# Kernel optimization log

Measured on AMD Instinct MI355X. Metric: run time of the kernel, lower is better.

## Reference

```python
import jax, jax.numpy as jnp
import numpy as np

DK, DV, NH = 512, 256, 8  # matches init_kwargs


def rel_to_abs(x):
    # x: (B, N, L, 2L-1) -> (B, N, L, L) via pad/reshape trick
    B, N, L, _ = x.shape
    x = jnp.pad(x, ((0, 0), (0, 0), (0, 0), (0, 1)))          # (B,N,L,2L)
    x = x.reshape(B, N, L * 2 * L)
    x = jnp.pad(x, ((0, 0), (0, 0), (0, L - 1)))
    x = x.reshape(B, N, L + 1, 2 * L - 1)
    return x[:, :, :L, L - 1:]


def relative_logits_1d(q, rel_k):
    # q: (B, nh, A, Wd, dkh); rel_k: (dkh, 2*Wd-1)
    B, nh, A, Wd, _ = q.shape
    rel = jnp.einsum('bnawc,cm->bnawm', q, rel_k)             # (B,nh,A,Wd,2Wd-1)
    rel = rel.reshape(B, nh * A, Wd, 2 * Wd - 1)
    rel = rel_to_abs(rel).reshape(B, nh, A, 1, Wd, Wd)
    return jnp.broadcast_to(rel, (B, nh, A, A, Wd, Wd))


def reference(x, w_qkv, w_conv, w_out, key_rel_h, key_rel_w):
    B, Cin, H, W = x.shape
    dkh, dvh = DK // NH, DV // NH
    L = H * W
    # 1x1 qkv projection (stride 1)
    qkv = jnp.einsum('bchw,oc->bohw', x, w_qkv)               # (B, 2dk+dv, H, W)
    q = qkv[:, :DK]
    k = qkv[:, DK:2 * DK]
    v = qkv[:, 2 * DK:]
    flat_q = q.reshape(B, NH, dkh, L) * (dkh ** -0.5)
    flat_k = k.reshape(B, NH, dkh, L)
    flat_v = v.reshape(B, NH, dvh, L)
    logits = jnp.einsum('bncs,bnct->bnst', flat_q, flat_k)     # (B,nh,L,L)
    # relative position logits (uses the already-scaled q, as in the torch code)
    qr = flat_q.reshape(B, NH, dkh, H, W).transpose(0, 1, 3, 4, 2)  # (B,nh,H,W,dkh)
    w_rel = relative_logits_1d(qr, key_rel_w)                  # (B,nh,H,H,W,W)
    h_rel = relative_logits_1d(qr.transpose(0, 1, 3, 2, 4), key_rel_h)  # (B,nh,W,W,H,H)
    h_rel = h_rel.transpose(0, 1, 2, 4, 3, 5).reshape(B, NH, L, L)
    w_rel = w_rel.transpose(0, 1, 4, 2, 5, 3).reshape(B, NH, L, L)
    logits = logits + h_rel + w_rel
    weights = jax.nn.softmax(logits, axis=-1)
    attn = jnp.einsum('bnst,bnct->bnsc', weights, flat_v)      # (B,nh,L,dvh)
    attn = attn.transpose(0, 1, 3, 2).reshape(B, DV, H, W)
    attn = jnp.einsum('bchw,oc->bohw', attn, w_out)            # 1x1 out_proj
    conv_out = jax.lax.conv_general_dilated(
        x, w_conv, window_strides=(1, 1), padding=[(1, 1), (1, 1)],
        dimension_numbers=('NCHW', 'OIHW', 'NCHW'))            # (B, out_c-dv, H, W)
    return jnp.concatenate([conv_out, attn], axis=1)


def setup_inputs() -> dict:
    key = jax.random.key(0)
    ks = jax.random.split(key, 6)
    H, W, Cin = 32, 32, 256
    return {
        'x': jax.random.normal(ks[0], (8, Cin, H, W), jnp.float32),
        'w_qkv': jax.random.normal(ks[1], (2 * DK + DV, Cin), jnp.float32) * 0.02,
        'w_conv': jax.random.normal(ks[2], (256, Cin, 3, 3), jnp.float32) * 0.02,
        'w_out': jax.random.normal(ks[3], (DV, DV), jnp.float32) * 0.02,
        'key_rel_h': DK ** -0.5 + jax.random.normal(ks[4], (DK // NH, 2 * H - 1), jnp.float32),
        'key_rel_w': DK ** -0.5 + jax.random.normal(ks[5], (DK // NH, 2 * W - 1), jnp.float32),
    }
```

## Files before the change

### kernel.cpp

```cpp
#include <hip/hip_runtime.h>
#include <cstddef>
#include <cstdint>

#define NB 8
#define CIN 256
#define LL 1024
#define DKC 512
#define DVC 256
#define XPSTRIDE 295936

typedef short short8 __attribute__((ext_vector_type(8)));
typedef float f32x4 __attribute__((ext_vector_type(4)));

__device__ __forceinline__ unsigned short f2bf(float f) {
  unsigned int u = __float_as_uint(f);
  u += 0x7fffu + ((u >> 16) & 1u);
  return (unsigned short)(u >> 16);
}
__device__ __forceinline__ float bf2f(unsigned short u) {
  return __uint_as_float(((unsigned int)u) << 16);
}

__global__ __launch_bounds__(256) void prep_weights(
    const float* __restrict__ wconv, const float* __restrict__ wqkv,
    const float* __restrict__ wout, const float* __restrict__ krh,
    const float* __restrict__ krw, unsigned short* __restrict__ wtap,
    unsigned short* __restrict__ wqbf, unsigned short* __restrict__ woutbf,
    unsigned short* __restrict__ relTh, unsigned short* __restrict__ relTw,
    unsigned short* __restrict__ xTp) {
  const int idx = blockIdx.x * 256 + threadIdx.x;
  if (idx < 589824) {
    const int g = idx >> 14;
    const int ot = g / 9, tap = g - ot * 9;
    const int rem2 = idx & 16383;
    const int kc = rem2 >> 12;
    const int row = (rem2 >> 6) & 63, kin = rem2 & 63;
    const int o = ot * 64 + row, c = kc * 64 + kin;
    wtap[idx] = f2bf(wconv[(size_t)(o * 256 + c) * 9 + tap]);
  } else if (idx < 917504) {
    const int j = idx - 589824;
    const int g = j >> 12;
    const int ot = g >> 2, kc = g & 3;
    const int row = (j >> 6) & 63, kin = j & 63;
    const int o = ot * 64 + row, c = kc * 64 + kin;
    const float sc = (o < DKC) ? 0.125f * 1.44269504088896f : 1.0f;
    wqbf[j] = f2bf(wqkv[o * 256 + c] * sc);
  } else if (idx < 983040) {
    const int j = idx - 917504;
    const int g = j >> 12;
    const int o = (g >> 2) * 64 + ((j >> 6) & 63);
    const int c = (g & 3) * 64 + (j & 63);
    woutbf[j] = f2bf(wout[o * 256 + c]);
  } else if (idx < 991232) {
    const int j = idx - 983040;
    const int tbl = j >> 12;
    const int rest = j & 4095;
    const int m = rest >> 6, c = rest & 63;
    const float* src = tbl ? krw : krh;
    unsigned short* dst = tbl ? relTw : relTh;
    const float v = (m < 63) ? src[c * 63 + m] : 0.f;
    dst[m * 64 + c] = f2bf(v);
  } else {
    const int j2 = idx - 991232;
    const int b = j2 / 33792;
    const int rem = j2 - b * 33792;
    const int pos = rem >> 8, c = rem & 255;
    int hp, wp;
    if (pos < 34) { hp = 0; wp = pos; }
    else if (pos < 68) { hp = 33; wp = pos - 34; }
    else if (pos < 100) { hp = pos - 68 + 1; wp = 0; }
    else { hp = pos - 100 + 1; wp = 33; }
    xTp[(size_t)b * XPSTRIDE + (hp * 34 + wp) * 256 + c] = 0;
  }
}

__global__ __launch_bounds__(256) void xpad_interior(
    const float* __restrict__ x, unsigned short* __restrict__ xTp) {
  __shared__ float tile[64][65];
  const int st = blockIdx.x;
  const int b = blockIdx.y;
  const int s0 = st * 64;
  const int h0 = st * 2;
  const int tid = threadIdx.x;
  for (int cc = 0; cc < 4; ++cc) {
    const int c0 = cc * 64;
    {
      const int row = tid >> 2;
      const int j0 = (tid & 3) * 16;
#pragma unroll
      for (int k = 0; k < 4; ++k)
        *(float4*)&tile[row][j0 + k * 4] =
            *(const float4*)(x + ((size_t)(b * CIN + c0 + row)) * LL + s0 + j0 + k * 4);
    }
    __syncthreads();
    {
      const int sl = tid >> 2;
      const int cb = (tid & 3) * 16;
      unsigned short buf[16];
#pragma unroll
      for (int m = 0; m < 16; ++m) buf[m] = f2bf(tile[cb + m][sl]);
      const int hp = h0 + (sl >> 5) + 1;
      const int wp = (sl & 31) + 1;
      unsigned short* dst = xTp + (size_t)b * XPSTRIDE + (hp * 34 + wp) * 256 + c0 + cb;
      *(uint4*)dst = *(uint4*)&buf[0];
      *(uint4*)(dst + 8) = *(uint4*)&buf[8];
    }
    __syncthreads();
  }
}

__global__ __launch_bounds__(256) void qkv_mfma(
    const unsigned short* __restrict__ xTp, const unsigned short* __restrict__ wqbf,
    unsigned short* __restrict__ qbf, unsigned short* __restrict__ kbf,
    unsigned short* __restrict__ vbf) {
  __shared__ __align__(16) char qsmem[16640];
  unsigned short* bs = (unsigned short*)qsmem;
  float (*trans)[65] = (float(*)[65])qsmem;
  const int tid = threadIdx.x;
  const int lane = tid & 63, w = tid >> 6;
  const int n16 = lane & 15, quad = lane >> 4;
  const int ot = blockIdx.x;
  const int st = blockIdx.y;
  const int b = blockIdx.z;
  const int s0 = st * 64;
  const int h0 = st * 2;
  const int trow = tid >> 3, ck = tid & 7;

  const unsigned short* xb = xTp + (size_t)b * XPSTRIDE;
  const unsigned short* wA = wqbf + (size_t)ot * 16384 + (w * 16 + n16) * 64 + quad * 8;
  const int wpos = (trow & 31) + 1;

  f32x4 acc[4];
#pragma unroll
  for (int nt = 0; nt < 4; ++nt) acc[nt] = (f32x4){0.f, 0.f, 0.f, 0.f};

  uint4 rb0 = *(const uint4*)(xb + (size_t)((h0 + 1) * 34 + wpos) * 256 + ck * 8);
  uint4 rb1 = *(const uint4*)(xb + (size_t)((h0 + 2) * 34 + wpos) * 256 + ck * 8);
  short8 af0 = *(const short8*)(wA);
  short8 af1 = *(const short8*)(wA + 32);
#pragma unroll
  for (int kc = 0; kc < 4; ++kc) {
    __syncthreads();
    *(uint4*)&bs[trow * 64 + ((ck ^ (trow & 7)) * 8)] = rb0;
    *(uint4*)&bs[(trow + 32) * 64 + ((ck ^ (trow & 7)) * 8)] = rb1;
    __syncthreads();
    short8 a0 = af0, a1 = af1;
    if (kc < 3) {
      const int c0 = (kc + 1) * 64;
      rb0 = *(const uint4*)(xb + (size_t)((h0 + 1) * 34 + wpos) * 256 + c0 + ck * 8);
      rb1 = *(const uint4*)(xb + (size_t)((h0 + 2) * 34 + wpos) * 256 + c0 + ck * 8);
      af0 = *(const short8*)(wA + (kc + 1) * 4096);
      af1 = *(const short8*)(wA + (kc + 1) * 4096 + 32);
    }
#pragma unroll
    for (int nt = 0; nt < 4; ++nt) {
      short8 b0 = *(const short8*)&bs[(nt * 16 + n16) * 64 + ((quad ^ (n16 & 7)) * 8)];
      short8 b1 = *(const short8*)&bs[(nt * 16 + n16) * 64 + (((quad + 4) ^ (n16 & 7)) * 8)];
      acc[nt] = __builtin_amdgcn_mfma_f32_16x16x32_bf16(a0, b0, acc[nt], 0, 0, 0);
      acc[nt] = __builtin_amdgcn_mfma_f32_16x16x32_bf16(a1, b1, acc[nt], 0, 0, 0);
    }
  }
  __syncthreads();
#pragma unroll
  for (int nt = 0; nt < 4; ++nt)
#pragma unroll
    for (int reg = 0; reg < 4; ++reg)
      trans[w * 16 + quad * 4 + reg][nt * 16 + n16] = acc[nt][reg];
  __syncthreads();
  const int sl = tid >> 2;
  const int cseg = (tid & 3) * 16;
  unsigned short buf[16];
  if (ot < 16) {
#pragma unroll
    for (int m = 0; m < 16; ++m) buf[m] = f2bf(trans[cseg + m][sl]);
    unsigned short* dst;
    int head;
    if (ot < 8) { dst = qbf; head = ot; }
    else { dst = kbf; head = ot - 8; }
    const size_t base = (((size_t)(b * 8 + head)) * LL + s0 + sl) * 64 + cseg;
    *(uint4*)(dst + base) = *(uint4*)&buf[0];
    *(uint4*)(dst + base + 8) = *(uint4*)&buf[8];
  } else {
#pragma unroll
    for (int m = 0; m < 16; ++m) buf[m] = f2bf(trans[sl][cseg + m]);
    unsigned short* dst = vbf + ((size_t)b * DVC + (ot - 16) * 64 + sl) * LL + s0 + cseg;
    *(uint4*)dst = *(uint4*)&buf[0];
    *(uint4*)(dst + 8) = *(uint4*)&buf[8];
  }
}

__global__ __launch_bounds__(256) void conv_mfma(
    const unsigned short* __restrict__ xTp, const unsigned short* __restrict__ wtap,
    float* __restrict__ out) {
  __shared__ __align__(16) unsigned short bs[64 * 64];
  const int tid = threadIdx.x;
  const int lane = tid & 63, w = tid >> 6;
  const int n16 = lane & 15, quad = lane >> 4;
  const int ot = blockIdx.x;
  const int st = blockIdx.y;
  const int b = blockIdx.z;
  const int s0 = st * 64;
  const int h0 = st * 2;
  const int trow = tid >> 3;
  const int ck = tid & 7;

  const unsigned short* xb = xTp + (size_t)b * XPSTRIDE;
  const unsigned short* wA = wtap + (size_t)ot * 147456 + (w * 16 + n16) * 64 + quad * 8;

  f32x4 acc[4];
#pragma unroll
  for (int nt = 0; nt < 4; ++nt) acc[nt] = (f32x4){0.f, 0.f, 0.f, 0.f};

  uint4 rb0, rb1;
  auto loadB = [&](int it) {
    const int tap = it >> 2;
    const int c0 = (it & 3) * 64;
    const int dh = tap / 3 - 1;
    const int dw = tap - (tap / 3) * 3 - 1;
    const int wp = (trow & 31) + dw + 1;
    rb0 = *(const uint4*)(xb + (size_t)((h0 + dh + 1) * 34 + wp) * 256 + c0 + ck * 8);
    rb1 = *(const uint4*)(xb + (size_t)((h0 + dh + 2) * 34 + wp) * 256 + c0 + ck * 8);
  };
  loadB(0);
  short8 af0 = *(const short8*)(wA);
  short8 af1 = *(const short8*)(wA + 32);
  for (int it = 0; it < 36; ++it) {
    __syncthreads();
    *(uint4*)&bs[trow * 64 + ((ck ^ (trow & 7)) * 8)] = rb0;
    *(uint4*)&bs[(trow + 32) * 64 + ((ck ^ (trow & 7)) * 8)] = rb1;
    __syncthreads();
    short8 a0 = af0, a1 = af1;
    if (it < 35) {
      loadB(it + 1);
      af0 = *(const short8*)(wA + (size_t)(it + 1) * 4096);
      af1 = *(const short8*)(wA + (size_t)(it + 1) * 4096 + 32);
    }
#pragma unroll
    for (int nt = 0; nt < 4; ++nt) {
      short8 b0 = *(const short8*)&bs[(nt * 16 + n16) * 64 + ((quad ^ (n16 & 7)) * 8)];
      short8 b1 = *(const short8*)&bs[(nt * 16 + n16) * 64 + (((quad + 4) ^ (n16 & 7)) * 8)];
      acc[nt] = __builtin_amdgcn_mfma_f32_16x16x32_bf16(a0, b0, acc[nt], 0, 0, 0);
      acc[nt] = __builtin_amdgcn_mfma_f32_16x16x32_bf16(a1, b1, acc[nt], 0, 0, 0);
    }
  }
#pragma unroll
  for (int nt = 0; nt < 4; ++nt)
#pragma unroll
    for (int reg = 0; reg < 4; ++reg)
      out[((size_t)b * 512 + ot * 64 + w * 16 + quad * 4 + reg) * LL + s0 + nt * 16 + n16] =
          acc[nt][reg];
}

__global__ __launch_bounds__(256, 4) void attn_kernel(
    const unsigned short* __restrict__ qbf, const unsigned short* __restrict__ kbf,
    const unsigned short* __restrict__ vbf, const unsigned short* __restrict__ relTh,
    const unsigned short* __restrict__ relTw, unsigned short* __restrict__ abf) {
  __shared__ __align__(16) char smem[28672];
  unsigned short* ks = (unsigned short*)smem;
  unsigned short* vs = (unsigned short*)(smem + 8192);
  unsigned short* ps = (unsigned short*)(smem + 12288);
  unsigned short* rwtT = (unsigned short*)(smem + 20480);
  float* obuf = (float*)smem;

  const int tid = threadIdx.x;
  const int lane = tid & 63, w = tid >> 6;
  const int n16 = lane & 15, quad = lane >> 4;
  const int blk = blockIdx.x;
  const int bn = blk & 63, qb = blk >> 6;
  const int n = bn & 7, b = bn >> 3;
  const int s0 = qb * 64;
  const int aa = 2 * qb + (w >> 1);
  const int pb = (w & 1) * 16;

  const unsigned short* qbase = qbf + ((size_t)(b * 8 + n)) * LL * 64;
  const unsigned short* kbase = kbf + ((size_t)(b * 8 + n)) * LL * 64;
  const unsigned short* vbase = vbf + ((size_t)(b * 8 + n)) * 32 * LL;

  const int ck = tid & 7;
  const int trow = tid >> 3;

  uint4 pk0 = *(const uint4*)(kbase + trow * 64 + ck * 8);
  uint4 pk1 = *(const uint4*)(kbase + (trow + 32) * 64 + ck * 8);
  uint4 pv = *(const uint4*)(vbase + (size_t)trow * LL + ck * 8);

  {
    const int sT = (pb + n16) * 32 + aa;
    short8 ra0 = *(const short8*)(qbase + (size_t)sT * 64 + quad * 8);
    short8 ra1 = *(const short8*)(qbase + (size_t)sT * 64 + 32 + quad * 8);
#pragma unroll
    for (int tbl = 0; tbl < 2; ++tbl) {
      const unsigned short* rel = tbl ? relTh : relTw;
      f32x4 acc[4];
#pragma unroll
      for (int mt = 0; mt < 4; ++mt) acc[mt] = (f32x4){0.f, 0.f, 0.f, 0.f};
#pragma unroll
      for (int mt = 0; mt < 4; ++mt) {
        short8 b0 = *(const short8*)(rel + (mt * 16 + n16) * 64 + quad * 8);
        short8 b1 = *(const short8*)(rel + (mt * 16 + n16) * 64 + 32 + quad * 8);
        acc[mt] = __builtin_amdgcn_mfma_f32_16x16x32_bf16(ra0, b0, acc[mt], 0, 0, 0);
        acc[mt] = __builtin_amdgcn_mfma_f32_16x16x32_bf16(ra1, b1, acc[mt], 0, 0, 0);
      }
      if (tbl == 0) {
#pragma unroll
        for (int mt = 0; mt < 4; ++mt)
#pragma unroll
          for (int reg = 0; reg < 4; ++reg)
            rwtT[(mt * 16 + n16) * 64 +
                 ((w * 16 + quad * 4 + reg) ^ ((n16 & 7) * 8))] = f2bf(acc[mt][reg]);
      } else {
#pragma unroll
        for (int mt = 0; mt < 4; ++mt)
#pragma unroll
          for (int reg = 0; reg < 4; ++reg)
            ps[(w * 16 + quad * 4 + reg) * 64 + mt * 16 + n16] = f2bf(acc[mt][reg]);
      }
    }
  }
  short8 qf0 = *(const short8*)(qbase + (size_t)(s0 + w * 16 + n16) * 64 + quad * 8);
  short8 qf1 = *(const short8*)(qbase + (size_t)(s0 + w * 16 + n16) * 64 + 32 + quad * 8);
  __syncthreads();
  float rhreg[2][4];
#pragma unroll
  for (int tt1 = 0; tt1 < 2; ++tt1)
#pragma unroll
    for (int reg = 0; reg < 4; ++reg) {
      const int iL = quad * 4 + reg;
      rhreg[tt1][reg] = bf2f(ps[(w * 16 + iL) * 64 + tt1 * 16 + n16 + 31 - pb - iL]);
    }

  float lacc[4] = {0.f, 0.f, 0.f, 0.f};
  f32x4 oacc[2];
  oacc[0] = (f32x4){0.f, 0.f, 0.f, 0.f};
  oacc[1] = (f32x4){0.f, 0.f, 0.f, 0.f};

  unsigned short* psw = ps + w * 1024;
  const int rb = w * 16 + quad * 4;

  for (int kt64 = 0; kt64 < 16; ++kt64) {
    const int t0 = kt64 * 64;
    __syncthreads();
    *(uint4*)&ks[trow * 64 + ((ck ^ (trow & 7)) * 8)] = pk0;
    *(uint4*)&ks[(trow + 32) * 64 + ((ck ^ (trow & 7)) * 8)] = pk1;
    *(uint4*)&vs[trow * 64 + ((ck ^ (trow & 7)) * 8)] = pv;
    __syncthreads();
    if (kt64 < 15) {
      const unsigned short* kg = kbase + (size_t)(t0 + 64) * 64;
      pk0 = *(const uint4*)(kg + trow * 64 + ck * 8);
      pk1 = *(const uint4*)(kg + (trow + 32) * 64 + ck * 8);
      pv = *(const uint4*)(vbase + (size_t)trow * LL + t0 + 64 + ck * 8);
    }

    f32x4 sacc[4];
#pragma unroll
    for (int tt = 0; tt < 4; ++tt) sacc[tt] = (f32x4){0.f, 0.f, 0.f, 0.f};
#pragma unroll
    for (int tt = 0; tt < 4; ++tt) {
      short8 kb0 = *(const short8*)&ks[(tt * 16 + n16) * 64 + ((quad ^ (n16 & 7)) * 8)];
      short8 kb1 = *(const short8*)&ks[(tt * 16 + n16) * 64 + (((quad + 4) ^ (n16 & 7)) * 8)];
      sacc[tt] = __builtin_amdgcn_mfma_f32_16x16x32_bf16(qf0, kb0, sacc[tt], 0, 0, 0);
      sacc[tt] = __builtin_amdgcn_mfma_f32_16x16x32_bf16(qf1, kb1, sacc[tt], 0, 0, 0);
    }
    float rwv[2][4];
#pragma unroll
    for (int h = 0; h < 2; ++h) {
      const int mw = (t0 >> 5) + h - aa + 31;
      const ushort4 rw4 = *(const ushort4*)&rwtT[mw * 64 + (rb ^ ((mw & 7) * 8))];
      rwv[h][0] = bf2f(rw4.x); rwv[h][1] = bf2f(rw4.y);
      rwv[h][2] = bf2f(rw4.z); rwv[h][3] = bf2f(rw4.w);
    }
#pragma unroll
    for (int tt = 0; tt < 4; ++tt)
#pragma unroll
      for (int reg = 0; reg < 4; ++reg) {
        const float e =
            __builtin_amdgcn_exp2f(sacc[tt][reg] + rwv[tt >> 1][reg] + rhreg[tt & 1][reg]);
        lacc[reg] += e;
        const int r = quad * 4 + reg;
        psw[r * 64 + (((tt * 2 + (n16 >> 3)) ^ (r & 7)) * 8) + (n16 & 7)] =
            (unsigned short)(__float_as_uint(e) >> 16);
      }
    __asm__ volatile("s_waitcnt lgkmcnt(0)" ::: "memory");
#pragma unroll
    for (int kt = 0; kt < 2; ++kt) {
      short8 pa = *(const short8*)&psw[n16 * 64 + (((quad + 4 * kt) ^ (n16 & 7)) * 8)];
#pragma unroll
      for (int ct = 0; ct < 2; ++ct) {
        short8 vb = *(const short8*)&vs[(ct * 16 + n16) * 64 + (((quad + 4 * kt) ^ (n16 & 7)) * 8)];
        oacc[ct] = __builtin_amdgcn_mfma_f32_16x16x32_bf16(pa, vb, oacc[ct], 0, 0, 0);
      }
    }
  }
  float linv[4];
#pragma unroll
  for (int reg = 0; reg < 4; ++reg) {
    float l = lacc[reg];
#pragma unroll
    for (int m = 1; m < 16; m <<= 1) l += __shfl_xor(l, m, 16);
    linv[reg] = 1.0f / l;
  }
  __syncthreads();
#pragma unroll
  for (int ct = 0; ct < 2; ++ct)
#pragma unroll
    for (int reg = 0; reg < 4; ++reg)
      obuf[(w * 16 + quad * 4 + reg) * 33 + ct * 16 + n16] = oacc[ct][reg] * linv[reg];
  __syncthreads();
  {
    const int row = tid >> 2;
    const int cseg = (tid & 3) * 8;
    unsigned short buf8[8];
#pragma unroll
    for (int m = 0; m < 8; ++m) buf8[m] = f2bf(obuf[row * 33 + cseg + m]);
    *(uint4*)(abf + (((size_t)b * LL) + s0 + row) * 256 + n * 32 + cseg) = *(uint4*)&buf8[0];
  }
}

__global__ __launch_bounds__(256) void proj_mfma(
    const unsigned short* __restrict__ abf, const unsigned short* __restrict__ woutbf,
    float* __restrict__ out) {
  __shared__ __align__(16) unsigned short bs[64 * 64];
  const int tid = threadIdx.x;
  const int lane = tid & 63, w = tid >> 6;
  const int n16 = lane & 15, quad = lane >> 4;
  const int ot = blockIdx.x;
  const int st = blockIdx.y;
  const int b = blockIdx.z;
  const int s0 = st * 64;
  const int trow = tid >> 3, ck = tid & 7;

  const unsigned short* ab = abf + ((size_t)b * LL + s0) * 256;
  const unsigned short* wA = woutbf + (size_t)ot * 16384 + (w * 16 + n16) * 64 + quad * 8;

  f32x4 acc[4];
#pragma unroll
  for (int nt = 0; nt < 4; ++nt) acc[nt] = (f32x4){0.f, 0.f, 0.f, 0.f};

  uint4 rb0 = *(const uint4*)(ab + (size_t)trow * 256 + ck * 8);
  uint4 rb1 = *(const uint4*)(ab + (size_t)(trow + 32) * 256 + ck * 8);
  short8 af0 = *(const short8*)(wA);
  short8 af1 = *(const short8*)(wA + 32);
#pragma unroll
  for (int kc = 0; kc < 4; ++kc) {
    __syncthreads();
    *(uint4*)&bs[trow * 64 + ((ck ^ (trow & 7)) * 8)] = rb0;
    *(uint4*)&bs[(trow + 32) * 64 + ((ck ^ (trow & 7)) * 8)] = rb1;
    __syncthreads();
    short8 a0 = af0, a1 = af1;
    if (kc < 3) {
      const int c0 = (kc + 1) * 64;
      rb0 = *(const uint4*)(ab + (size_t)trow * 256 + c0 + ck * 8);
      rb1 = *(const uint4*)(ab + (size_t)(trow + 32) * 256 + c0 + ck * 8);
      af0 = *(const short8*)(wA + (kc + 1) * 4096);
      af1 = *(const short8*)(wA + (kc + 1) * 4096 + 32);
    }
#pragma unroll
    for (int nt = 0; nt < 4; ++nt) {
      short8 b0 = *(const short8*)&bs[(nt * 16 + n16) * 64 + ((quad ^ (n16 & 7)) * 8)];
      short8 b1 = *(const short8*)&bs[(nt * 16 + n16) * 64 + (((quad + 4) ^ (n16 & 7)) * 8)];
      acc[nt] = __builtin_amdgcn_mfma_f32_16x16x32_bf16(a0, b0, acc[nt], 0, 0, 0);
      acc[nt] = __builtin_amdgcn_mfma_f32_16x16x32_bf16(a1, b1, acc[nt], 0, 0, 0);
    }
  }
#pragma unroll
  for (int nt = 0; nt < 4; ++nt)
#pragma unroll
    for (int reg = 0; reg < 4; ++reg)
      out[((size_t)b * 512 + 256 + ot * 64 + w * 16 + quad * 4 + reg) * LL + s0 + nt * 16 + n16] =
          acc[nt][reg];
}

extern "C" void kernel_launch(void* const* d_in, const int* in_sizes, int n_in,
                              void* d_out, int out_size, void* d_ws, size_t ws_size,
                              hipStream_t stream) {
  const float* x     = (const float*)d_in[0];
  const float* wqkv  = (const float*)d_in[1];
  const float* wconv = (const float*)d_in[2];
  const float* wout  = (const float*)d_in[3];
  const float* krh   = (const float*)d_in[4];
  const float* krw   = (const float*)d_in[5];
  float* out = (float*)d_out;

  unsigned short* qbf = (unsigned short*)d_ws;
  unsigned short* kbf = qbf + (size_t)NB * 8 * LL * 64;
  unsigned short* vbf = kbf + (size_t)NB * 8 * LL * 64;
  unsigned short* abf = vbf + (size_t)NB * DVC * LL;
  unsigned short* relTh = abf + (size_t)NB * LL * DVC;
  unsigned short* relTw = relTh + 4096;
  unsigned short* xTp = relTw + 4096;
  unsigned short* wtap = xTp + (size_t)NB * XPSTRIDE;
  unsigned short* wqbf = wtap + 589824;
  unsigned short* woutbf = wqbf + 327680;

  prep_weights<<<dim3(4928), 256, 0, stream>>>(wconv, wqkv, wout, krh, krw,
                                               wtap, wqbf, woutbf, relTh, relTw, xTp);
  xpad_interior<<<dim3(16, 8), 256, 0, stream>>>(x, xTp);
  qkv_mfma<<<dim3(20, 16, NB), 256, 0, stream>>>(xTp, wqbf, qbf, kbf, vbf);
  conv_mfma<<<dim3(4, 16, NB), 256, 0, stream>>>(xTp, wtap, out);
  attn_kernel<<<dim3(1024), 256, 0, stream>>>(qbf, kbf, vbf, relTh, relTw, abf);
  proj_mfma<<<dim3(4, 16, NB), 256, 0, stream>>>(abf, woutbf, out);
}
```

Measured before the change: 162.7 us.

## Double attention query tile per block and merge input prep kernels

Each attention block now handles 128 query rows instead of 64. K/V tiles loaded into shared memory are reused across two row sets, and the grid shrinks to 512 blocks. Shared memory grows and the occupancy hint drops from 4 to 2 blocks per CU, trading parallelism and registers for fewer K/V reloads. Separately, the x padding/transpose kernel is folded into the weight prep kernel to save one launch.

```diff
diff --git a/kernel.cpp b/kernel.cpp
--- a/kernel.cpp
+++ b/kernel.cpp
@@ -21,14 +21,48 @@
   return __uint_as_float(((unsigned int)u) << 16);
 }
 
-__global__ __launch_bounds__(256) void prep_weights(
-    const float* __restrict__ wconv, const float* __restrict__ wqkv,
-    const float* __restrict__ wout, const float* __restrict__ krh,
-    const float* __restrict__ krw, unsigned short* __restrict__ wtap,
-    unsigned short* __restrict__ wqbf, unsigned short* __restrict__ woutbf,
-    unsigned short* __restrict__ relTh, unsigned short* __restrict__ relTw,
-    unsigned short* __restrict__ xTp) {
-  const int idx = blockIdx.x * 256 + threadIdx.x;
+__global__ __launch_bounds__(256) void prep_all(
+    const float* __restrict__ x, const float* __restrict__ wconv,
+    const float* __restrict__ wqkv, const float* __restrict__ wout,
+    const float* __restrict__ krh, const float* __restrict__ krw,
+    unsigned short* __restrict__ wtap, unsigned short* __restrict__ wqbf,
+    unsigned short* __restrict__ woutbf, unsigned short* __restrict__ relTh,
+    unsigned short* __restrict__ relTw, unsigned short* __restrict__ xTp) {
+  __shared__ float tile[64][65];
+  const int tid = threadIdx.x;
+  if (blockIdx.x < 128) {
+    const int st = blockIdx.x & 15;
+    const int b = blockIdx.x >> 4;
+    const int s0 = st * 64;
+    const int h0 = st * 2;
+    for (int cc = 0; cc < 4; ++cc) {
+      const int c0 = cc * 64;
+      {
+        const int row = tid >> 2;
+        const int j0 = (tid & 3) * 16;
+#pragma unroll
+        for (int k = 0; k < 4; ++k)
+          *(float4*)&tile[row][j0 + k * 4] =
+              *(const float4*)(x + ((size_t)(b * CIN + c0 + row)) * LL + s0 + j0 + k * 4);
+      }
+      __syncthreads();
+      {
+        const int sl = tid >> 2;
+        const int cb = (tid & 3) * 16;
+        unsigned short buf[16];
+#pragma unroll
+        for (int m = 0; m < 16; ++m) buf[m] = f2bf(tile[cb + m][sl]);
+        const int hp = h0 + (sl >> 5) + 1;
+        const int wp = (sl & 31) + 1;
+        unsigned short* dst = xTp + (size_t)b * XPSTRIDE + (hp * 34 + wp) * 256 + c0 + cb;
+        *(uint4*)dst = *(uint4*)&buf[0];
+        *(uint4*)(dst + 8) = *(uint4*)&buf[8];
+      }
+      __syncthreads();
+    }
+    return;
+  }
+  const int idx = (blockIdx.x - 128) * 256 + tid;
   if (idx < 589824) {
     const int g = idx >> 14;
     const int ot = g / 9, tap = g - ot * 9;
@@ -74,41 +108,6 @@
   }
 }
 
-__global__ __launch_bounds__(256) void xpad_interior(
-    const float* __restrict__ x, unsigned short* __restrict__ xTp) {
-  __shared__ float tile[64][65];
-  const int st = blockIdx.x;
-  const int b = blockIdx.y;
-  const int s0 = st * 64;
-  const int h0 = st * 2;
-  const int tid = threadIdx.x;
-  for (int cc = 0; cc < 4; ++cc) {
-    const int c0 = cc * 64;
-    {
-      const int row = tid >> 2;
-      const int j0 = (tid & 3) * 16;
-#pragma unroll
-      for (int k = 0; k < 4; ++k)
-        *(float4*)&tile[row][j0 + k * 4] =
-            *(const float4*)(x + ((size_t)(b * CIN + c0 + row)) * LL + s0 + j0 + k * 4);
-    }
-    __syncthreads();
-    {
-      const int sl = tid >> 2;
-      const int cb = (tid & 3) * 16;
-      unsigned short buf[16];
-#pragma unroll
-      for (int m = 0; m < 16; ++m) buf[m] = f2bf(tile[cb + m][sl]);
-      const int hp = h0 + (sl >> 5) + 1;
-      const int wp = (sl & 31) + 1;
-      unsigned short* dst = xTp + (size_t)b * XPSTRIDE + (hp * 34 + wp) * 256 + c0 + cb;
-      *(uint4*)dst = *(uint4*)&buf[0];
-      *(uint4*)(dst + 8) = *(uint4*)&buf[8];
-    }
-    __syncthreads();
-  }
-}
-
 __global__ __launch_bounds__(256) void qkv_mfma(
     const unsigned short* __restrict__ xTp, const unsigned short* __restrict__ wqbf,
     unsigned short* __restrict__ qbf, unsigned short* __restrict__ kbf,
@@ -251,26 +250,26 @@
           acc[nt][reg];
 }
 
-__global__ __launch_bounds__(256, 4) void attn_kernel(
+__global__ __launch_bounds__(256, 2) void attn_kernel(
     const unsigned short* __restrict__ qbf, const unsigned short* __restrict__ kbf,
     const unsigned short* __restrict__ vbf, const unsigned short* __restrict__ relTh,
     const unsigned short* __restrict__ relTw, unsigned short* __restrict__ abf) {
-  __shared__ __align__(16) char smem[28672];
+  __shared__ __align__(16) char smem[45056];
   unsigned short* ks = (unsigned short*)smem;
   unsigned short* vs = (unsigned short*)(smem + 8192);
   unsigned short* ps = (unsigned short*)(smem + 12288);
-  unsigned short* rwtT = (unsigned short*)(smem + 20480);
+  unsigned short* rwtT = (unsigned short*)(smem + 28672);
   float* obuf = (float*)smem;
 
   const int tid = threadIdx.x;
   const int lane = tid & 63, w = tid >> 6;
   const int n16 = lane & 15, quad = lane >> 4;
   const int blk = blockIdx.x;
-  const int bn = blk & 63, qb = blk >> 6;
+  const int bn = blk & 63, qt = blk >> 6;
   const int n = bn & 7, b = bn >> 3;
-  const int s0 = qb * 64;
-  const int aa = 2 * qb + (w >> 1);
+  const int s0 = qt * 128;
   const int pb = (w & 1) * 16;
+  const int aar[2] = {4 * qt + (w >> 1), 4 * qt + 2 + (w >> 1)};
 
   const unsigned short* qbase = qbf + ((size_t)(b * 8 + n)) * LL * 64;
   const unsigned short* kbase = kbf + ((size_t)(b * 8 + n)) * LL * 64;
@@ -283,7 +282,9 @@
   uint4 pk1 = *(const uint4*)(kbase + (trow + 32) * 64 + ck * 8);
   uint4 pv = *(const uint4*)(vbase + (size_t)trow * LL + ck * 8);
 
-  {
+#pragma unroll
+  for (int rs = 0; rs < 2; ++rs) {
+    const int aa = aar[rs];
     const int sT = (pb + n16) * 32 + aa;
     short8 ra0 = *(const short8*)(qbase + (size_t)sT * 64 + quad * 8);
     short8 ra1 = *(const short8*)(qbase + (size_t)sT * 64 + 32 + quad * 8);
@@ -305,36 +306,45 @@
         for (int mt = 0; mt < 4; ++mt)
 #pragma unroll
           for (int reg = 0; reg < 4; ++reg)
-            rwtT[(mt * 16 + n16) * 64 +
-                 ((w * 16 + quad * 4 + reg) ^ ((n16 & 7) * 8))] = f2bf(acc[mt][reg]);
+            rwtT[(mt * 16 + n16) * 128 +
+                 ((rs * 64 + w * 16 + quad * 4 + reg) ^ ((n16 & 7) * 8))] = f2bf(acc[mt][reg]);
       } else {
 #pragma unroll
         for (int mt = 0; mt < 4; ++mt)
 #pragma unroll
           for (int reg = 0; reg < 4; ++reg)
-            ps[(w * 16 + quad * 4 + reg) * 64 + mt * 16 + n16] = f2bf(acc[mt][reg]);
-      }
-    }
-  }
-  short8 qf0 = *(const short8*)(qbase + (size_t)(s0 + w * 16 + n16) * 64 + quad * 8);
-  short8 qf1 = *(const short8*)(qbase + (size_t)(s0 + w * 16 + n16) * 64 + 32 + quad * 8);
+            ps[(rs * 64 + w * 16 + quad * 4 + reg) * 64 + mt * 16 + n16] = f2bf(acc[mt][reg]);
+      }
+    }
+  }
+  short8 qf[2][2];
+#pragma unroll
+  for (int rs = 0; rs < 2; ++rs) {
+    const size_t qrow = (size_t)(s0 + rs * 64 + w * 16 + n16) * 64;
+    qf[rs][0] = *(const short8*)(qbase + qrow + quad * 8);
+    qf[rs][1] = *(const short8*)(qbase + qrow + 32 + quad * 8);
+  }
   __syncthreads();
-  float rhreg[2][4];
-#pragma unroll
-  for (int tt1 = 0; tt1 < 2; ++tt1)
-#pragma unroll
-    for (int reg = 0; reg < 4; ++reg) {
-      const int iL = quad * 4 + reg;
-      rhreg[tt1][reg] = bf2f(ps[(w * 16 + iL) * 64 + tt1 * 16 + n16 + 31 - pb - iL]);
-    }
-
-  float lacc[4] = {0.f, 0.f, 0.f, 0.f};
-  f32x4 oacc[2];
-  oacc[0] = (f32x4){0.f, 0.f, 0.f, 0.f};
-  oacc[1] = (f32x4){0.f, 0.f, 0.f, 0.f};
-
-  unsigned short* psw = ps + w * 1024;
-  const int rb = w * 16 + quad * 4;
+  float rhreg[2][2][4];
+#pragma unroll
+  for (int rs = 0; rs < 2; ++rs)
+#pragma unroll
+    for (int tt1 = 0; tt1 < 2; ++tt1)
+#pragma unroll
+      for (int reg = 0; reg < 4; ++reg) {
+        const int iL = quad * 4 + reg;
+        rhreg[rs][tt1][reg] =
+            bf2f(ps[(rs * 64 + w * 16 + iL) * 64 + tt1 * 16 + n16 + 31 - pb - iL]);
+      }
+
+  float lacc[2][4] = {};
+  f32x4 oacc[2][2];
+#pragma unroll
+  for (int rs = 0; rs < 2; ++rs)
+#pragma unroll
+    for (int ct = 0; ct < 2; ++ct) oacc[rs][ct] = (f32x4){0.f, 0.f, 0.f, 0.f};
+
+  const int rbq = w * 16 + quad * 4;
 
   for (int kt64 = 0; kt64 < 16; ++kt64) {
     const int t0 = kt64 * 64;
@@ -350,68 +360,91 @@
       pv = *(const uint4*)(vbase + (size_t)trow * LL + t0 + 64 + ck * 8);
     }
 
-    f32x4 sacc[4];
-#pragma unroll
-    for (int tt = 0; tt < 4; ++tt) sacc[tt] = (f32x4){0.f, 0.f, 0.f, 0.f};
+    f32x4 sacc[2][4];
+#pragma unroll
+    for (int rs = 0; rs < 2; ++rs)
+#pragma unroll
+      for (int tt = 0; tt < 4; ++tt) sacc[rs][tt] = (f32x4){0.f, 0.f, 0.f, 0.f};
 #pragma unroll
     for (int tt = 0; tt < 4; ++tt) {
       short8 kb0 = *(const short8*)&ks[(tt * 16 + n16) * 64 + ((quad ^ (n16 & 7)) * 8)];
       short8 kb1 = *(const short8*)&ks[(tt * 16 + n16) * 64 + (((quad + 4) ^ (n16 & 7)) * 8)];
-      sacc[tt] = __builtin_amdgcn_mfma_f32_16x16x32_bf16(qf0, kb0, sacc[tt], 0, 0, 0);
-      sacc[tt] = __builtin_amdgcn_mfma_f32_16x16x32_bf16(qf1, kb1, sacc[tt], 0, 0, 0);
-    }
-    float rwv[2][4];
-#pragma unroll
-    for (int h = 0; h < 2; ++h) {
-      const int mw = (t0 >> 5) + h - aa + 31;
-      const ushort4 rw4 = *(const ushort4*)&rwtT[mw * 64 + (rb ^ ((mw & 7) * 8))];
-      rwv[h][0] = bf2f(rw4.x); rwv[h][1] = bf2f(rw4.y);
-      rwv[h][2] = bf2f(rw4.z); rwv[h][3] = bf2f(rw4.w);
-    }
-#pragma unroll
-    for (int tt = 0; tt < 4; ++tt)
-#pragma unroll
-      for (int reg = 0; reg < 4; ++reg) {
-        const float e =
-            __builtin_amdgcn_exp2f(sacc[tt][reg] + rwv[tt >> 1][reg] + rhreg[tt & 1][reg]);
-        lacc[reg] += e;
-        const int r = quad * 4 + reg;
-        psw[r * 64 + (((tt * 2 + (n16 >> 3)) ^ (r & 7)) * 8) + (n16 & 7)] =
-            (unsigned short)(__float_as_uint(e) >> 16);
-      }
+#pragma unroll
+      for (int rs = 0; rs < 2; ++rs) {
+        sacc[rs][tt] = __builtin_amdgcn_mfma_f32_16x16x32_bf16(qf[rs][0], kb0, sacc[rs][tt], 0, 0, 0);
+        sacc[rs][tt] = __builtin_amdgcn_mfma_f32_16x16x32_bf16(qf[rs][1], kb1, sacc[rs][tt], 0, 0, 0);
+      }
+    }
+    float rwv[2][2][4];
+#pragma unroll
+    for (int rs = 0; rs < 2; ++rs)
+#pragma unroll
+      for (int h = 0; h < 2; ++h) {
+        const int mw = (t0 >> 5) + h - aar[rs] + 31;
+        const ushort4 rw4 =
+            *(const ushort4*)&rwtT[mw * 128 + ((rs * 64 + rbq) ^ ((mw & 7) * 8))];
+        rwv[rs][h][0] = bf2f(rw4.x); rwv[rs][h][1] = bf2f(rw4.y);
+        rwv[rs][h][2] = bf2f(rw4.z); rwv[rs][h][3] = bf2f(rw4.w);
+      }
+#pragma unroll
+    for (int rs = 0; rs < 2; ++rs)
+#pragma unroll
+      for (int tt = 0; tt < 4; ++tt)
+#pragma unroll
+        for (int reg = 0; reg < 4; ++reg) {
+          const float e = __builtin_amdgcn_exp2f(sacc[rs][tt][reg] + rwv[rs][tt >> 1][reg] +
+                                                 rhreg[rs][tt & 1][reg]);
+          lacc[rs][reg] += e;
+          const int r = quad * 4 + reg;
+          ps[(rs * 64 + w * 16 + r) * 64 + (((tt * 2 + (n16 >> 3)) ^ (r & 7)) * 8) + (n16 & 7)] =
+              (unsigned short)(__float_as_uint(e) >> 16);
+        }
     __asm__ volatile("s_waitcnt lgkmcnt(0)" ::: "memory");
 #pragma unroll
     for (int kt = 0; kt < 2; ++kt) {
-      short8 pa = *(const short8*)&psw[n16 * 64 + (((quad + 4 * kt) ^ (n16 & 7)) * 8)];
+      short8 pa[2];
+#pragma unroll
+      for (int rs = 0; rs < 2; ++rs)
+        pa[rs] = *(const short8*)&ps[(rs * 64 + w * 16 + n16) * 64 +
+                                     (((quad + 4 * kt) ^ (n16 & 7)) * 8)];
 #pragma unroll
       for (int ct = 0; ct < 2; ++ct) {
         short8 vb = *(const short8*)&vs[(ct * 16 + n16) * 64 + (((quad + 4 * kt) ^ (n16 & 7)) * 8)];
-        oacc[ct] = __builtin_amdgcn_mfma_f32_16x16x32_bf16(pa, vb, oacc[ct], 0, 0, 0);
-      }
-    }
-  }
-  float linv[4];
-#pragma unroll
-  for (int reg = 0; reg < 4; ++reg) {
-    float l = lacc[reg];
-#pragma unroll
-    for (int m = 1; m < 16; m <<= 1) l += __shfl_xor(l, m, 16);
-    linv[reg] = 1.0f / l;
-  }
+#pragma unroll
+        for (int rs = 0; rs < 2; ++rs)
+          oacc[rs][ct] = __builtin_amdgcn_mfma_f32_16x16x32_bf16(pa[rs], vb, oacc[rs][ct], 0, 0, 0);
+      }
+    }
+  }
+  float linv[2][4];
+#pragma unroll
+  for (int rs = 0; rs < 2; ++rs)
+#pragma unroll
+    for (int reg = 0; reg < 4; ++reg) {
+      float l = lacc[rs][reg];
+#pragma unroll
+      for (int m = 1; m < 16; m <<= 1) l += __shfl_xor(l, m, 16);
+      linv[rs][reg] = 1.0f / l;
+    }
   __syncthreads();
 #pragma unroll
-  for (int ct = 0; ct < 2; ++ct)
-#pragma unroll
-    for (int reg = 0; reg < 4; ++reg)
-      obuf[(w * 16 + quad * 4 + reg) * 33 + ct * 16 + n16] = oacc[ct][reg] * linv[reg];
+  for (int rs = 0; rs < 2; ++rs)
+#pragma unroll
+    for (int ct = 0; ct < 2; ++ct)
+#pragma unroll
+      for (int reg = 0; reg < 4; ++reg)
+        obuf[(rs * 64 + w * 16 + quad * 4 + reg) * 33 + ct * 16 + n16] =
+            oacc[rs][ct][reg] * linv[rs][reg];
   __syncthreads();
   {
-    const int row = tid >> 2;
-    const int cseg = (tid & 3) * 8;
-    unsigned short buf8[8];
-#pragma unroll
-    for (int m = 0; m < 8; ++m) buf8[m] = f2bf(obuf[row * 33 + cseg + m]);
-    *(uint4*)(abf + (((size_t)b * LL) + s0 + row) * 256 + n * 32 + cseg) = *(uint4*)&buf8[0];
+    const int row = tid >> 1;
+    const int cseg = (tid & 1) * 16;
+    unsigned short buf16[16];
+#pragma unroll
+    for (int m = 0; m < 16; ++m) buf16[m] = f2bf(obuf[row * 33 + cseg + m]);
+    unsigned short* dst = abf + (((size_t)b * LL) + s0 + row) * 256 + n * 32 + cseg;
+    *(uint4*)dst = *(uint4*)&buf16[0];
+    *(uint4*)(dst + 8) = *(uint4*)&buf16[8];
   }
 }
 
@@ -491,11 +524,10 @@
   unsigned short* wqbf = wtap + 589824;
   unsigned short* woutbf = wqbf + 327680;
 
-  prep_weights<<<dim3(4928), 256, 0, stream>>>(wconv, wqkv, wout, krh, krw,
-                                               wtap, wqbf, woutbf, relTh, relTw, xTp);
-  xpad_interior<<<dim3(16, 8), 256, 0, stream>>>(x, xTp);
+  prep_all<<<dim3(5056), 256, 0, stream>>>(x, wconv, wqkv, wout, krh, krw,
+                                           wtap, wqbf, woutbf, relTh, relTw, xTp);
   qkv_mfma<<<dim3(20, 16, NB), 256, 0, stream>>>(xTp, wqbf, qbf, kbf, vbf);
   conv_mfma<<<dim3(4, 16, NB), 256, 0, stream>>>(xTp, wtap, out);
-  attn_kernel<<<dim3(1024), 256, 0, stream>>>(qbf, kbf, vbf, relTh, relTw, abf);
+  attn_kernel<<<dim3(512), 256, 0, stream>>>(qbf, kbf, vbf, relTh, relTw, abf);
   proj_mfma<<<dim3(4, 16, NB), 256, 0, stream>>>(abf, woutbf, out);
 }
```

Measured after the change: 161.8 us (median of 2 runs). No clear change (-0.6%).
